# Optimization experiments

Hardware: AMD Instinct MI355X
Metric: run time of the kernel (lower is better)

## Reference

```python
import jax, jax.numpy as jnp
import numpy as np

TWO_PI = 6.283185  # constant used verbatim in the original module


def setup_inputs() -> dict:
    key = jax.random.key(0)
    ks = jax.random.split(key, 12)
    N, input_size, light_freq, H = 8388608, 11, 16, 16
    d_in = input_size - 2 + 2 * light_freq  # 41
    x = jax.random.uniform(ks[0], (N, input_size), dtype=jnp.float32)
    B_light = jax.random.normal(ks[1], (2, light_freq), dtype=jnp.float32)
    W1 = jax.random.normal(ks[2], (d_in, H), dtype=jnp.float32) * (1.0 / np.sqrt(d_in))
    b1 = jax.random.normal(ks[3], (H,), dtype=jnp.float32) * 0.01
    W2 = jax.random.normal(ks[4], (H, H), dtype=jnp.float32) * 0.25
    b2 = jax.random.normal(ks[5], (H,), dtype=jnp.float32) * 0.01
    W3 = jax.random.normal(ks[6], (H, H), dtype=jnp.float32) * 0.25
    b3 = jax.random.normal(ks[7], (H,), dtype=jnp.float32) * 0.01
    W4 = jax.random.normal(ks[8], (H, H), dtype=jnp.float32) * 0.25
    b4 = jax.random.normal(ks[9], (H,), dtype=jnp.float32) * 0.01
    W5 = jax.random.normal(ks[10], (H, 1), dtype=jnp.float32) * 0.25
    b5 = jax.random.normal(ks[11], (1,), dtype=jnp.float32) * 0.01
    return {"x": x, "B_light": B_light, "W1": W1, "b1": b1, "W2": W2, "b2": b2,
            "W3": W3, "b3": b3, "W4": W4, "b4": b4, "W5": W5, "b5": b5}


def reference(x, B_light, W1, b1, W2, b2, W3, b3, W4, b4, W5, b5):
    # Fourier-feature encoding of the last two input dims (light direction)
    x_light = TWO_PI * (x[:, -2:] @ B_light)                      # [N, F]
    feats = jnp.concatenate([x[:, :-2], jnp.cos(x_light), jnp.sin(x_light)], axis=-1)  # [N, 41]
    # Tiny 5-layer MLP with ELU activations
    h = jax.nn.elu(feats @ W1 + b1)
    h = jax.nn.elu(h @ W2 + b2)
    h = jax.nn.elu(h @ W3 + b3)
    h = jax.nn.elu(h @ W4 + b4)
    out = h @ W5 + b5                                             # [N, 1]
    return out
```

## Files before the change

kernel.cpp:

```cpp
#include <hip/hip_runtime.h>

typedef __fp16   cvt16x2 __attribute__((ext_vector_type(2)));
typedef _Float16 h2      __attribute__((ext_vector_type(2)));
typedef _Float16 half4_t __attribute__((ext_vector_type(4)));
typedef unsigned uint2v  __attribute__((ext_vector_type(2)));
typedef float    f32x4   __attribute__((ext_vector_type(4)));

#define CH 4

#if !__has_builtin(__builtin_elementwise_exp2)
extern "C" __device__ _Float16 __ocml_exp2_f16(_Float16);
#endif

__device__ __forceinline__ unsigned pk(float a, float b) {
    cvt16x2 h = __builtin_amdgcn_cvt_pkrtz(a, b);
    return __builtin_bit_cast(unsigned, h);
}
__device__ __forceinline__ half4_t mkfrag(unsigned lo, unsigned hi) {
    uint2v u; u[0] = lo; u[1] = hi;
    return __builtin_bit_cast(half4_t, u);
}

__device__ __forceinline__ unsigned elu_pk(float a, float b) {
    h2 v = __builtin_bit_cast(h2, __builtin_amdgcn_cvt_pkrtz(a, b));
    const h2 z  = {(_Float16)0.f, (_Float16)0.f};
    const h2 lg = {(_Float16)1.44269504f, (_Float16)1.44269504f};
    const h2 m1 = {(_Float16)-1.f, (_Float16)-1.f};
    h2 mx = __builtin_elementwise_max(v, z);
    h2 mn = __builtin_elementwise_min(v, z);
    h2 tt = mn * lg;
#if __has_builtin(__builtin_elementwise_exp2)
    h2 ev = __builtin_elementwise_exp2(tt);
#else
    h2 ev; ev[0] = __ocml_exp2_f16(tt[0]); ev[1] = __ocml_exp2_f16(tt[1]);
#endif
    h2 r = mx + (ev + m1);
    return __builtin_bit_cast(unsigned, r);
}

__global__ __launch_bounds__(128, 4) void pixenc_mfma4(
    const float* __restrict__ x,
    const float* __restrict__ Bl,
    const float* __restrict__ W1, const float* __restrict__ b1,
    const float* __restrict__ W2, const float* __restrict__ b2,
    const float* __restrict__ W3, const float* __restrict__ b3,
    const float* __restrict__ W4, const float* __restrict__ b4,
    const float* __restrict__ W5, const float* __restrict__ b5,
    float* __restrict__ out, int N)
{
    const int t    = threadIdx.x;
    const int lane = t & 63;
    const int w    = t >> 6;
    const int g    = lane >> 4;
    const int m    = lane & 15;

    half4_t A1[3], A2, A3, A4;
    #pragma unroll
    for (int e = 0; e < 4; ++e) {
        const int c0 = 4 * e + g;
        A1[0][e] = (c0 < 9) ? (_Float16)W1[c0 * 16 + m] : (_Float16)0.f;
        A1[1][e] = (_Float16)W1[(9  + g * 4 + e) * 16 + m];
        A1[2][e] = (_Float16)W1[(25 + g * 4 + e) * 16 + m];
        A2[e]    = (_Float16)W2[(g * 4 + e) * 16 + m];
        A3[e]    = (_Float16)W3[(g * 4 + e) * 16 + m];
        A4[e]    = (_Float16)W4[(g * 4 + e) * 16 + m];
    }
    f32x4 c1, c2, c3, c4;
    float w5v[4], blc[4], bls[4];
    #pragma unroll
    for (int e = 0; e < 4; ++e) {
        const int r = g * 4 + e;
        c1[e] = b1[r]; c2[e] = b2[r]; c3[e] = b3[r]; c4[e] = b4[r];
        w5v[e] = W5[r];
        blc[e] = Bl[r]; bls[e] = Bl[16 + r];
    }
    const float b5v = b5[0];

    const int wavebase = blockIdx.x * (128 * CH) + w * (64 * CH);

    for (int c = 0; c < CH; ++c) {
        const int sbase = wavebase + c * 64;

        float xg0[4], xg1[4], x8v[4], x9v[4], x10v[4];
        #pragma unroll
        for (int s = 0; s < 4; ++s) {
            int j = sbase + s * 16 + m; if (j >= N) j = N - 1;
            const float* rb = x + (size_t)j * 11;
            xg0[s] = rb[g];  xg1[s] = rb[4 + g];
            x8v[s] = rb[8];  x9v[s] = rb[9];  x10v[s] = rb[10];
        }

        half4_t F0[4], F1[4], F2[4];
        #pragma unroll
        for (int s = 0; s < 4; ++s) {
            float cs[4], sn[4];
            #pragma unroll
            for (int e = 0; e < 4; ++e) {
                float zz = fmaf(x9v[s], blc[e], x10v[s] * bls[e]);
                zz = __builtin_amdgcn_fractf(zz);
                cs[e] = __builtin_amdgcn_cosf(zz);
                sn[e] = __builtin_amdgcn_sinf(zz);
            }
            F0[s] = mkfrag(pk(xg0[s], xg1[s]), pk(x8v[s], 0.f));
            F1[s] = mkfrag(pk(cs[0], cs[1]), pk(cs[2], cs[3]));
            F2[s] = mkfrag(pk(sn[0], sn[1]), pk(sn[2], sn[3]));
        }

        f32x4 acc[4];
        #pragma unroll
        for (int s = 0; s < 4; ++s) acc[s] = c1;
        #pragma unroll
        for (int s = 0; s < 4; ++s)
            acc[s] = __builtin_amdgcn_mfma_f32_16x16x16f16(A1[0], F0[s], acc[s], 0, 0, 0);
        #pragma unroll
        for (int s = 0; s < 4; ++s)
            acc[s] = __builtin_amdgcn_mfma_f32_16x16x16f16(A1[1], F1[s], acc[s], 0, 0, 0);
        #pragma unroll
        for (int s = 0; s < 4; ++s)
            acc[s] = __builtin_amdgcn_mfma_f32_16x16x16f16(A1[2], F2[s], acc[s], 0, 0, 0);

        half4_t H[4];
        #pragma unroll
        for (int s = 0; s < 4; ++s)
            H[s] = mkfrag(elu_pk(acc[s][0], acc[s][1]), elu_pk(acc[s][2], acc[s][3]));
        #pragma unroll
        for (int s = 0; s < 4; ++s)
            acc[s] = __builtin_amdgcn_mfma_f32_16x16x16f16(A2, H[s], c2, 0, 0, 0);

        #pragma unroll
        for (int s = 0; s < 4; ++s)
            H[s] = mkfrag(elu_pk(acc[s][0], acc[s][1]), elu_pk(acc[s][2], acc[s][3]));
        #pragma unroll
        for (int s = 0; s < 4; ++s)
            acc[s] = __builtin_amdgcn_mfma_f32_16x16x16f16(A3, H[s], c3, 0, 0, 0);

        #pragma unroll
        for (int s = 0; s < 4; ++s)
            H[s] = mkfrag(elu_pk(acc[s][0], acc[s][1]), elu_pk(acc[s][2], acc[s][3]));
        #pragma unroll
        for (int s = 0; s < 4; ++s)
            acc[s] = __builtin_amdgcn_mfma_f32_16x16x16f16(A4, H[s], c4, 0, 0, 0);

        #pragma unroll
        for (int s = 0; s < 4; ++s) {
            float p = 0.f;
            #pragma unroll
            for (int e = 0; e < 4; ++e) {
                const float v = acc[s][e];
                const float el = v > 0.f ? v : __expf(v) - 1.f;
                p = fmaf(el, w5v[e], p);
            }
            p += __shfl_xor(p, 16, 64);
            p += __shfl_xor(p, 32, 64);
            const int o = sbase + s * 16 + m;
            if (g == 0 && o < N) out[o] = p + b5v;
        }
    }
}

extern "C" void kernel_launch(void* const* d_in, const int* in_sizes, int n_in,
                              void* d_out, int out_size, void* d_ws, size_t ws_size,
                              hipStream_t stream) {
    const float* x  = (const float*)d_in[0];
    const float* Bl = (const float*)d_in[1];
    const float* W1 = (const float*)d_in[2];
    const float* b1 = (const float*)d_in[3];
    const float* W2 = (const float*)d_in[4];
    const float* b2 = (const float*)d_in[5];
    const float* W3 = (const float*)d_in[6];
    const float* b3 = (const float*)d_in[7];
    const float* W4 = (const float*)d_in[8];
    const float* b4 = (const float*)d_in[9];
    const float* W5 = (const float*)d_in[10];
    const float* b5 = (const float*)d_in[11];
    float* out = (float*)d_out;

    const int N = out_size;
    const int blocks = (N + 128 * CH - 1) / (128 * CH);
    pixenc_mfma4<<<blocks, 128, 0, stream>>>(x, Bl, W1, b1, W2, b2, W3, b3,
                                             W4, b4, W5, b5, out, N);
}
```

Measured before the change: 146.6 us.

## Prefetch next chunk's inputs, interleave layer-1 MFMAs, use fp16 dot for final layer

Loads the input rows for the next 64-sample chunk into registers before computing the current one, so global-load latency overlaps the MFMA and transcendental work. The first-layer fragment build and its three MFMAs are now interleaved per sub-tile instead of issued in separate phases. The last layer applies packed fp16 ELU and a dot2 instruction instead of scalar fp32 exp and FMAs. This costs extra registers for the prefetched values under the 4-waves launch bound, and lowers the final-layer activation to fp16 precision.

```diff
diff --git a/kernel.cpp b/kernel.cpp
--- a/kernel.cpp
+++ b/kernel.cpp
@@ -38,7 +38,17 @@
     return __builtin_bit_cast(unsigned, r);
 }
 
-__global__ __launch_bounds__(128, 4) void pixenc_mfma4(
+__device__ __forceinline__ float hdot2(unsigned a, unsigned b, float c) {
+#if __has_builtin(__builtin_amdgcn_fdot2)
+    return __builtin_amdgcn_fdot2(__builtin_bit_cast(cvt16x2, a),
+                                  __builtin_bit_cast(cvt16x2, b), c, false);
+#else
+    h2 av = __builtin_bit_cast(h2, a), bv = __builtin_bit_cast(h2, b);
+    return fmaf((float)av[1], (float)bv[1], fmaf((float)av[0], (float)bv[0], c));
+#endif
+}
+
+__global__ __launch_bounds__(128, 4) void pixenc_mfma5(
     const float* __restrict__ x,
     const float* __restrict__ Bl,
     const float* __restrict__ W1, const float* __restrict__ b1,
@@ -66,31 +76,44 @@
         A4[e]    = (_Float16)W4[(g * 4 + e) * 16 + m];
     }
     f32x4 c1, c2, c3, c4;
-    float w5v[4], blc[4], bls[4];
+    float blc[4], bls[4];
     #pragma unroll
     for (int e = 0; e < 4; ++e) {
         const int r = g * 4 + e;
         c1[e] = b1[r]; c2[e] = b2[r]; c3[e] = b3[r]; c4[e] = b4[r];
-        w5v[e] = W5[r];
         blc[e] = Bl[r]; bls[e] = Bl[16 + r];
     }
+    const unsigned w5p0 = pk(W5[g * 4 + 0], W5[g * 4 + 1]);
+    const unsigned w5p1 = pk(W5[g * 4 + 2], W5[g * 4 + 3]);
     const float b5v = b5[0];
 
     const int wavebase = blockIdx.x * (128 * CH) + w * (64 * CH);
 
+    float xg0[4], xg1[4], x8v[4], x9v[4], x10v[4];
+    #pragma unroll
+    for (int s = 0; s < 4; ++s) {
+        int j = wavebase + s * 16 + m; if (j >= N) j = N - 1;
+        const float* rb = x + (size_t)j * 11;
+        xg0[s] = rb[g];  xg1[s] = rb[4 + g];
+        x8v[s] = rb[8];  x9v[s] = rb[9];  x10v[s] = rb[10];
+    }
+
+    #pragma unroll
     for (int c = 0; c < CH; ++c) {
         const int sbase = wavebase + c * 64;
 
-        float xg0[4], xg1[4], x8v[4], x9v[4], x10v[4];
-        #pragma unroll
-        for (int s = 0; s < 4; ++s) {
-            int j = sbase + s * 16 + m; if (j >= N) j = N - 1;
-            const float* rb = x + (size_t)j * 11;
-            xg0[s] = rb[g];  xg1[s] = rb[4 + g];
-            x8v[s] = rb[8];  x9v[s] = rb[9];  x10v[s] = rb[10];
-        }
-
-        half4_t F0[4], F1[4], F2[4];
+        float ng0[4], ng1[4], n8[4], n9[4], n10[4];
+        if (c + 1 < CH) {
+            #pragma unroll
+            for (int s = 0; s < 4; ++s) {
+                int j = sbase + 64 + s * 16 + m; if (j >= N) j = N - 1;
+                const float* rb = x + (size_t)j * 11;
+                ng0[s] = rb[g];  ng1[s] = rb[4 + g];
+                n8[s]  = rb[8];  n9[s]  = rb[9];  n10[s] = rb[10];
+            }
+        }
+
+        f32x4 acc[4];
         #pragma unroll
         for (int s = 0; s < 4; ++s) {
             float cs[4], sn[4];
@@ -101,23 +124,15 @@
                 cs[e] = __builtin_amdgcn_cosf(zz);
                 sn[e] = __builtin_amdgcn_sinf(zz);
             }
-            F0[s] = mkfrag(pk(xg0[s], xg1[s]), pk(x8v[s], 0.f));
-            F1[s] = mkfrag(pk(cs[0], cs[1]), pk(cs[2], cs[3]));
-            F2[s] = mkfrag(pk(sn[0], sn[1]), pk(sn[2], sn[3]));
-        }
-
-        f32x4 acc[4];
-        #pragma unroll
-        for (int s = 0; s < 4; ++s) acc[s] = c1;
-        #pragma unroll
-        for (int s = 0; s < 4; ++s)
-            acc[s] = __builtin_amdgcn_mfma_f32_16x16x16f16(A1[0], F0[s], acc[s], 0, 0, 0);
-        #pragma unroll
-        for (int s = 0; s < 4; ++s)
-            acc[s] = __builtin_amdgcn_mfma_f32_16x16x16f16(A1[1], F1[s], acc[s], 0, 0, 0);
-        #pragma unroll
-        for (int s = 0; s < 4; ++s)
-            acc[s] = __builtin_amdgcn_mfma_f32_16x16x16f16(A1[2], F2[s], acc[s], 0, 0, 0);
+            const half4_t F0 = mkfrag(pk(xg0[s], xg1[s]), pk(x8v[s], 0.f));
+            const half4_t F1 = mkfrag(pk(cs[0], cs[1]), pk(cs[2], cs[3]));
+            const half4_t F2 = mkfrag(pk(sn[0], sn[1]), pk(sn[2], sn[3]));
+            f32x4 a = c1;
+            a = __builtin_amdgcn_mfma_f32_16x16x16f16(A1[0], F0, a, 0, 0, 0);
+            a = __builtin_amdgcn_mfma_f32_16x16x16f16(A1[1], F1, a, 0, 0, 0);
+            a = __builtin_amdgcn_mfma_f32_16x16x16f16(A1[2], F2, a, 0, 0, 0);
+            acc[s] = a;
+        }
 
         half4_t H[4];
         #pragma unroll
@@ -143,17 +158,21 @@
 
         #pragma unroll
         for (int s = 0; s < 4; ++s) {
-            float p = 0.f;
-            #pragma unroll
-            for (int e = 0; e < 4; ++e) {
-                const float v = acc[s][e];
-                const float el = v > 0.f ? v : __expf(v) - 1.f;
-                p = fmaf(el, w5v[e], p);
-            }
+            const unsigned u0 = elu_pk(acc[s][0], acc[s][1]);
+            const unsigned u1 = elu_pk(acc[s][2], acc[s][3]);
+            float p = hdot2(u1, w5p1, hdot2(u0, w5p0, 0.f));
             p += __shfl_xor(p, 16, 64);
             p += __shfl_xor(p, 32, 64);
             const int o = sbase + s * 16 + m;
             if (g == 0 && o < N) out[o] = p + b5v;
+        }
+
+        if (c + 1 < CH) {
+            #pragma unroll
+            for (int s = 0; s < 4; ++s) {
+                xg0[s] = ng0[s]; xg1[s] = ng1[s];
+                x8v[s] = n8[s];  x9v[s] = n9[s];  x10v[s] = n10[s];
+            }
         }
     }
 }
@@ -177,6 +196,6 @@
 
     const int N = out_size;
     const int blocks = (N + 128 * CH - 1) / (128 * CH);
-    pixenc_mfma4<<<blocks, 128, 0, stream>>>(x, Bl, W1, b1, W2, b2, W3, b3,
+    pixenc_mfma5<<<blocks, 128, 0, stream>>>(x, Bl, W1, b1, W2, b2, W3, b3,
                                              W4, b4, W5, b5, out, N);
 }
```

Result: no change. 144.9 us (-1.2%).
